# Kernel optimization log

Measured on AMD Instinct MI355X. Metric: run time of the kernel, lower is better.

Reference implementation:

```python
import jax, jax.numpy as jnp
import numpy as np

N_FEAT = 1024
N_HIDDEN = 31


def _lstm_cell(x, h, c, W_ih, W_hh, b_ih, b_hh):
    # PyTorch LSTMCell: gates ordered i, f, g, o
    gates = x @ W_ih.T + b_ih + h @ W_hh.T + b_hh
    i, f, g, o = jnp.split(gates, 4, axis=-1)
    i = jax.nn.sigmoid(i)
    f = jax.nn.sigmoid(f)
    g = jnp.tanh(g)
    o = jax.nn.sigmoid(o)
    c_new = f * c + i * g
    h_new = o * jnp.tanh(c_new)
    return h_new, c_new


def setup_inputs() -> dict:
    key = jax.random.key(0)
    ks = jax.random.split(key, 12)
    B, T = 64, 512
    s1 = 1.0 / np.sqrt(N_HIDDEN)
    inp = {
        "input": jax.random.normal(ks[0], (B, T, N_FEAT), dtype=jnp.float32),
        "W_ih1": jax.random.uniform(ks[1], (4 * N_HIDDEN, N_FEAT), jnp.float32, -s1, s1),
        "W_hh1": jax.random.uniform(ks[2], (4 * N_HIDDEN, N_HIDDEN), jnp.float32, -s1, s1),
        "b_ih1": jax.random.uniform(ks[3], (4 * N_HIDDEN,), jnp.float32, -s1, s1),
        "b_hh1": jax.random.uniform(ks[4], (4 * N_HIDDEN,), jnp.float32, -s1, s1),
        "W_ih2": jax.random.uniform(ks[5], (4 * N_HIDDEN, N_HIDDEN), jnp.float32, -s1, s1),
        "W_hh2": jax.random.uniform(ks[6], (4 * N_HIDDEN, N_HIDDEN), jnp.float32, -s1, s1),
        "b_ih2": jax.random.uniform(ks[7], (4 * N_HIDDEN,), jnp.float32, -s1, s1),
        "b_hh2": jax.random.uniform(ks[8], (4 * N_HIDDEN,), jnp.float32, -s1, s1),
        "W_lin": jax.random.uniform(ks[9], (N_FEAT, N_HIDDEN), jnp.float32, -s1, s1),
        "b_lin": jax.random.uniform(ks[10], (N_FEAT,), jnp.float32, -s1, s1),
        "future": 16,
    }
    return inp


def reference(input, W_ih1, W_hh1, b_ih1, b_hh1, W_ih2, W_hh2, b_ih2, b_hh2, W_lin, b_lin, future):
    B = input.shape[0]
    h0 = jnp.zeros((B, N_HIDDEN), dtype=input.dtype)
    state0 = (h0, h0, h0, h0)  # h_t, c_t, h_t2, c_t2

    def step(state, x_t):
        h_t, c_t, h_t2, c_t2 = state
        h_t, c_t = _lstm_cell(x_t, h_t, c_t, W_ih1, W_hh1, b_ih1, b_hh1)
        h_t2, c_t2 = _lstm_cell(h_t, h_t2, c_t2, W_ih2, W_hh2, b_ih2, b_hh2)
        out = h_t2 @ W_lin.T + b_lin  # [B, N_FEAT]
        return (h_t, c_t, h_t2, c_t2), out

    # teacher-forced pass over the given sequence
    xs = jnp.swapaxes(input, 0, 1)  # [T, B, F]
    state, outs = jax.lax.scan(step, state0, xs)
    last = outs[-1]

    def fut_step(carry, _):
        state, out = carry
        state, out = step(state, out)
        return (state, out), out

    if future > 0:
        _, fut_outs = jax.lax.scan(fut_step, (state, last), None, length=future)
        outs = jnp.concatenate([outs, fut_outs], axis=0)

    return jnp.swapaxes(outs, 0, 1)  # [B, T+future, N_FEAT]
```

## Files before the change

kernel.cpp:

```cpp
#include <hip/hip_runtime.h>
#include <hip/hip_bf16.h>

#define BB_  64
#define TT_  512
#define FF_  1024
#define HH_  31
#define GG_  124
#define FUT_ 16
#define TTOT_ 528
#define OUT_ROW_ ((size_t)TTOT_ * FF_)

#define PRE1_OFF ((size_t)0)
#define H2A_OFF  (PRE1_OFF + (size_t)TT_*64*128)
#define WT_OFF   (H2A_OFF  + (size_t)TTOT_*64*32)
#define MV_OFF   (WT_OFF   + 31*1024)

__device__ __forceinline__ float rdlane(float v, int k) {
    return __uint_as_float(__builtin_amdgcn_readlane(__float_as_uint(v), k));
}

#define REP31(M) M(0) M(1) M(2) M(3) M(4) M(5) M(6) M(7) M(8) M(9) \
                 M(10) M(11) M(12) M(13) M(14) M(15) M(16) M(17) M(18) M(19) \
                 M(20) M(21) M(22) M(23) M(24) M(25) M(26) M(27) M(28) M(29) M(30)
#define REP16E(M) M(0) M(2) M(4) M(6) M(8) M(10) M(12) M(14) \
                  M(16) M(18) M(20) M(22) M(24) M(26) M(28) M(30)
#define REP15O(M) M(1) M(3) M(5) M(7) M(9) M(11) M(13) M(15) \
                  M(17) M(19) M(21) M(23) M(25) M(27) M(29)

__global__ __launch_bounds__(256) void k_front(
    const float* __restrict__ X,
    const float* __restrict__ Wih1,
    const float* __restrict__ bih1,
    const float* __restrict__ bhh1,
    const float* __restrict__ Wlin,
    const float* __restrict__ blin,
    float* __restrict__ pre1,
    float* __restrict__ WT,
    float* __restrict__ Mv)
{
    __shared__ __align__(16) float xs[32][128];
    __shared__ __align__(16) float ws[32][128];
    const int blk = blockIdx.x;
    const int tid = threadIdx.x;

    if (blk < 256) {
        const int t0   = blk * 2;
        const int tcol = tid & 15, trow = tid >> 4;
        const int c0 = tcol * 8, r0 = trow * 8;

        float4 a0[8], a1[8];
#pragma unroll
        for (int r = 0; r < 8; r++) { a0[r] = make_float4(0.f,0.f,0.f,0.f); a1[r] = a0[r]; }

        for (int kc = 0; kc < 32; ++kc) {
            const int k0f = kc * 32;
#pragma unroll
            for (int p = 0; p < 4; p++) {
                int i = tid + p * 256;
                int r = i >> 3, f = i & 7;
                int bb = r & 63, tt = t0 + (r >> 6);
                float4 v = *(const float4*)(X + (size_t)bb * TT_ * FF_ + (size_t)tt * FF_ + k0f + f * 4);
                xs[f * 4 + 0][r] = v.x; xs[f * 4 + 1][r] = v.y;
                xs[f * 4 + 2][r] = v.z; xs[f * 4 + 3][r] = v.w;
            }
#pragma unroll
            for (int p = 0; p < 4; p++) {
                int i = tid + p * 256;
                int g = i >> 3, f = i & 7;
                float4 v = make_float4(0.f, 0.f, 0.f, 0.f);
                if (g < GG_) v = *(const float4*)(Wih1 + (size_t)g * FF_ + k0f + f * 4);
                ws[f * 4 + 0][g] = v.x; ws[f * 4 + 1][g] = v.y;
                ws[f * 4 + 2][g] = v.z; ws[f * 4 + 3][g] = v.w;
            }
            __syncthreads();
#pragma unroll
            for (int k = 0; k < 32; k++) {
                float4 wv0 = *(const float4*)&ws[k][c0];
                float4 wv1 = *(const float4*)&ws[k][c0 + 4];
                float4 xa  = *(const float4*)&xs[k][r0];
                float4 xb  = *(const float4*)&xs[k][r0 + 4];
                float rx[8] = {xa.x, xa.y, xa.z, xa.w, xb.x, xb.y, xb.z, xb.w};
#pragma unroll
                for (int r = 0; r < 8; r++) {
                    a0[r].x += rx[r] * wv0.x; a0[r].y += rx[r] * wv0.y;
                    a0[r].z += rx[r] * wv0.z; a0[r].w += rx[r] * wv0.w;
                    a1[r].x += rx[r] * wv1.x; a1[r].y += rx[r] * wv1.y;
                    a1[r].z += rx[r] * wv1.z; a1[r].w += rx[r] * wv1.w;
                }
            }
            __syncthreads();
        }
        float bias0[4], bias1[4];
#pragma unroll
        for (int cc = 0; cc < 4; cc++) {
            int c = c0 + cc;
            bias0[cc] = (c < GG_) ? (bih1[c] + bhh1[c]) : 0.0f;
            c = c0 + 4 + cc;
            bias1[cc] = (c < GG_) ? (bih1[c] + bhh1[c]) : 0.0f;
        }
#pragma unroll
        for (int r = 0; r < 8; r++) {
            int row = r0 + r;
            int m = (t0 + (row >> 6)) * 64 + (row & 63);
            float4 o0 = a0[r], o1 = a1[r];
            o0.x += bias0[0]; o0.y += bias0[1]; o0.z += bias0[2]; o0.w += bias0[3];
            o1.x += bias1[0]; o1.y += bias1[1]; o1.z += bias1[2]; o1.w += bias1[3];
            *(float4*)(pre1 + (size_t)m * 128 + c0)     = o0;
            *(float4*)(pre1 + (size_t)m * 128 + c0 + 4) = o1;
        }
    } else if (blk < 380) {
        int i = (blk - 256) * 256 + tid;
        int j = i / 31;
        int k = i - j * 31;
        WT[k * 1024 + j] = Wlin[i];
    } else {
        int idx = (blk - 380) * 256 + tid;
        if (idx < GG_ * 32) {
            int g = idx >> 5, k = idx & 31;
            const float* wr = Wih1 + (size_t)g * FF_;
            float acc = 0.0f;
            if (k < 31) {
#pragma unroll 8
                for (int j = 0; j < FF_; j++) acc += wr[j] * Wlin[j * 31 + k];
            } else {
#pragma unroll 8
                for (int j = 0; j < FF_; j++) acc += wr[j] * blin[j];
            }
            Mv[idx] = acc;
        }
    }
}

__global__ __attribute__((amdgpu_flat_work_group_size(128, 128), amdgpu_waves_per_eu(1)))
void k2_recur(
    const float* __restrict__ pre1,
    const float* __restrict__ Whh1,
    const float* __restrict__ Wih2,
    const float* __restrict__ Whh2,
    const float* __restrict__ bih1, const float* __restrict__ bhh1,
    const float* __restrict__ bih2, const float* __restrict__ bhh2,
    const float* __restrict__ Mv,
    float* __restrict__ h2a)
{
    __shared__ float gA[2][128];
    __shared__ float g2[2][128];
    const int L  = threadIdx.x;
    const int bb = blockIdx.x;
    const int j  = L & 63;
    const int gc = (L < GG_) ? L : (GG_ - 1);
    const bool isg = (gc >= 62 && gc < 93);
    const bool selhi = (j >= 32);
    const int sidx = selhi ? (j - 32) : j;

#define WLOAD(k) float w1_##k  = Whh1[gc * 31 + k]; \
                 float wi2_##k = Wih2[gc * 31 + k]; \
                 float wh2_##k = Whh2[gc * 31 + k];
    REP31(WLOAD)
#undef WLOAD
#define WPIN(k) asm("" : "+v"(w1_##k), "+v"(wi2_##k), "+v"(wh2_##k));
    REP31(WPIN)
#undef WPIN

    const float b2c = bih2[gc] + bhh2[gc];

    float hv = 0.0f, cv = 0.0f;

    float cur0 = pre1[(size_t)bb * 128 + L];
    float pnxt = pre1[((size_t)1 * 64 + bb) * 128 + L];
    float pnx2 = pre1[((size_t)2 * 64 + bb) * 128 + L];
    {
        float pa0 = cur0, pa1 = 0.0f;
#define DPE(k) { float hk = rdlane(hv, 32 + k); pa0 += w1_##k * hk; }
#define DPO(k) { float hk = rdlane(hv, 32 + k); pa1 += w1_##k * hk; }
        REP16E(DPE)
        REP15O(DPO)
#undef DPE
#undef DPO
        float a = pa0 + pa1;
        float z = isg ? (2.0f * a) : a;
        float s = 1.0f / (1.0f + __expf(-z));
        gA[1][L] = isg ? (2.0f * s - 1.0f) : s;
    }
    __syncthreads();
    {
        const float* gsrc = &gA[1][0];
        float ig = gsrc[sidx];
        float fg = gsrc[sidx + 31];
        float gg = gsrc[sidx + 62];
        float og = gsrc[sidx + 93];
        float cvn = fg * cv + ig * gg;
        float e = __expf(-2.0f * cvn);
        float hvn = og * (2.0f / (1.0f + e) - 1.0f);
        cv = selhi ? cvn : 0.0f;
        hv = selhi ? hvn : 0.0f;
    }

    for (int t = 0; t < TT_ - 1; t++) {
        const int pb = t & 1;
        const float cur = pnxt;
        pnxt = pnx2;
        if (t + 3 < TT_) pnx2 = pre1[((size_t)(t + 3) * 64 + bb) * 128 + L];

        float bi0 = b2c, bi1 = 0.0f, bh0 = 0.0f, bh1 = 0.0f;
        float pa0 = cur, pa1 = 0.0f;
#define DME(k) { float h1k = rdlane(hv, 32 + k); float h2k = rdlane(hv, k); \
                 bi0 += wi2_##k * h1k; bh0 += wh2_##k * h2k; pa0 += w1_##k * h1k; }
#define DMO(k) { float h1k = rdlane(hv, 32 + k); float h2k = rdlane(hv, k); \
                 bi1 += wi2_##k * h1k; bh1 += wh2_##k * h2k; pa1 += w1_##k * h1k; }
        REP16E(DME)
        REP15O(DMO)
#undef DME
#undef DMO
        float b = (bi0 + bi1) + (bh0 + bh1);
        float a = pa0 + pa1;
        {
            float z = isg ? (2.0f * b) : b;
            float s = 1.0f / (1.0f + __expf(-z));
            g2[pb][L] = isg ? (2.0f * s - 1.0f) : s;
        }
        {
            float z = isg ? (2.0f * a) : a;
            float s = 1.0f / (1.0f + __expf(-z));
            gA[pb][L] = isg ? (2.0f * s - 1.0f) : s;
        }
        __syncthreads();
        {
            const float* gsrc = selhi ? &gA[pb][0] : &g2[pb][0];
            float ig = gsrc[sidx];
            float fg = gsrc[sidx + 31];
            float gg = gsrc[sidx + 62];
            float og = gsrc[sidx + 93];
            cv = fg * cv + ig * gg;
            float e = __expf(-2.0f * cv);
            hv = og * (2.0f / (1.0f + e) - 1.0f);
        }
        if (L < HH_) h2a[((size_t)t * 64 + bb) * 32 + L] = hv;
    }

    {
        float bi0 = b2c, bi1 = 0.0f, bh0 = 0.0f, bh1 = 0.0f;
#define DTE(k) { float h1k = rdlane(hv, 32 + k); float h2k = rdlane(hv, k); \
                 bi0 += wi2_##k * h1k; bh0 += wh2_##k * h2k; }
#define DTO(k) { float h1k = rdlane(hv, 32 + k); float h2k = rdlane(hv, k); \
                 bi1 += wi2_##k * h1k; bh1 += wh2_##k * h2k; }
        REP16E(DTE)
        REP15O(DTO)
#undef DTE
#undef DTO
        float b = (bi0 + bi1) + (bh0 + bh1);
        float z = isg ? (2.0f * b) : b;
        float s = 1.0f / (1.0f + __expf(-z));
        g2[1][L] = isg ? (2.0f * s - 1.0f) : s;
    }
    __syncthreads();
    {
        const float* gsrc = &g2[1][0];
        float ig = gsrc[sidx];
        float fg = gsrc[sidx + 31];
        float gg = gsrc[sidx + 62];
        float og = gsrc[sidx + 93];
        float cvn = fg * cv + ig * gg;
        float e = __expf(-2.0f * cvn);
        float hvn = og * (2.0f / (1.0f + e) - 1.0f);
        cv = selhi ? cv : cvn;
        hv = selhi ? hv : hvn;
    }
    if (L < HH_) h2a[((size_t)(TT_ - 1) * 64 + bb) * 32 + L] = hv;

#define MLOAD(k) float m_##k = Mv[gc * 32 + k];
    REP31(MLOAD)
#undef MLOAD
    float m_31 = Mv[gc * 32 + 31];
#define MPIN(k) asm("" : "+v"(m_##k));
    REP31(MPIN)
#undef MPIN
    asm("" : "+v"(m_31));
    const float b1c = bih1[gc] + bhh1[gc];

    for (int sft = 0; sft < FUT_; sft++) {
        float pa0 = b1c + m_31, pa1 = 0.0f;
#define DFE(k) { float h2k = rdlane(hv, k); pa0 += m_##k * h2k; }
#define DFO(k) { float h2k = rdlane(hv, k); pa1 += m_##k * h2k; }
        REP16E(DFE)
        REP15O(DFO)
#undef DFE
#undef DFO
#define DGE(k) { float h1k = rdlane(hv, 32 + k); pa0 += w1_##k * h1k; }
#define DGO(k) { float h1k = rdlane(hv, 32 + k); pa1 += w1_##k * h1k; }
        REP16E(DGE)
        REP15O(DGO)
#undef DGE
#undef DGO
        {
            float a = pa0 + pa1;
            float z = isg ? (2.0f * a) : a;
            float s = 1.0f / (1.0f + __expf(-z));
            gA[0][L] = isg ? (2.0f * s - 1.0f) : s;
        }
        __syncthreads();
        {
            const float* gsrc = &gA[0][0];
            float ig = gsrc[sidx];
            float fg = gsrc[sidx + 31];
            float gg = gsrc[sidx + 62];
            float og = gsrc[sidx + 93];
            float cvn = fg * cv + ig * gg;
            float e = __expf(-2.0f * cvn);
            float hvn = og * (2.0f / (1.0f + e) - 1.0f);
            cv = selhi ? cvn : cv;
            hv = selhi ? hvn : hv;
        }
        float bi0 = b2c, bi1 = 0.0f, bh0 = 0.0f, bh1 = 0.0f;
#define DHE(k) { float h1k = rdlane(hv, 32 + k); float h2k = rdlane(hv, k); \
                 bi0 += wi2_##k * h1k; bh0 += wh2_##k * h2k; }
#define DHO(k) { float h1k = rdlane(hv, 32 + k); float h2k = rdlane(hv, k); \
                 bi1 += wi2_##k * h1k; bh1 += wh2_##k * h2k; }
        REP16E(DHE)
        REP15O(DHO)
#undef DHE
#undef DHO
        {
            float b = (bi0 + bi1) + (bh0 + bh1);
            float z = isg ? (2.0f * b) : b;
            float s = 1.0f / (1.0f + __expf(-z));
            g2[0][L] = isg ? (2.0f * s - 1.0f) : s;
        }
        __syncthreads();
        {
            const float* gsrc = &g2[0][0];
            float ig = gsrc[sidx];
            float fg = gsrc[sidx + 31];
            float gg = gsrc[sidx + 62];
            float og = gsrc[sidx + 93];
            float cvn = fg * cv + ig * gg;
            float e = __expf(-2.0f * cvn);
            float hvn = og * (2.0f / (1.0f + e) - 1.0f);
            cv = selhi ? cv : cvn;
            hv = selhi ? hv : hvn;
        }
        if (L < HH_) h2a[((size_t)(TT_ + sft) * 64 + bb) * 32 + L] = hv;
    }
}

__global__ __launch_bounds__(256) void k3_outlin(
    const float* __restrict__ h2a,
    const float* __restrict__ WT,
    const float* __restrict__ blin,
    float* __restrict__ out)
{
    __shared__ __align__(16) float hl[32][32];
    const int tid = threadIdx.x;
    const int m0  = blockIdx.x * 32;
#pragma unroll
    for (int p = 0; p < 4; p++) {
        int i = tid + p * 256;
        int r = i >> 5, k = i & 31;
        hl[r][k] = h2a[(size_t)(m0 + r) * 32 + k];
    }
    __syncthreads();
    const int c0 = tid * 4;
    float4 bl = *(const float4*)(blin + c0);
    float4 acc[32];
#pragma unroll
    for (int r = 0; r < 32; r++) acc[r] = bl;
    for (int k = 0; k < 31; k++) {
        float4 wv = *(const float4*)(WT + k * 1024 + c0);
#pragma unroll
        for (int r = 0; r < 32; r++) {
            float h = hl[r][k];
            acc[r].x += h * wv.x; acc[r].y += h * wv.y;
            acc[r].z += h * wv.z; acc[r].w += h * wv.w;
        }
    }
    const int t  = m0 >> 6;
    const int b0 = m0 & 63;
#pragma unroll
    for (int r = 0; r < 32; r++) {
        int b = b0 + r;
        *(float4*)(out + (size_t)b * OUT_ROW_ + (size_t)t * FF_ + c0) = acc[r];
    }
}

extern "C" void kernel_launch(void* const* d_in, const int* in_sizes, int n_in,
                              void* d_out, int out_size, void* d_ws, size_t ws_size,
                              hipStream_t stream) {
    (void)in_sizes; (void)n_in; (void)out_size; (void)ws_size;
    const float* X    = (const float*)d_in[0];
    const float* Wih1 = (const float*)d_in[1];
    const float* Whh1 = (const float*)d_in[2];
    const float* bih1 = (const float*)d_in[3];
    const float* bhh1 = (const float*)d_in[4];
    const float* Wih2 = (const float*)d_in[5];
    const float* Whh2 = (const float*)d_in[6];
    const float* bih2 = (const float*)d_in[7];
    const float* bhh2 = (const float*)d_in[8];
    const float* Wlin = (const float*)d_in[9];
    const float* blin = (const float*)d_in[10];

    float* ws   = (float*)d_ws;
    float* pre1 = ws + PRE1_OFF;
    float* h2a  = ws + H2A_OFF;
    float* WT   = ws + WT_OFF;
    float* Mv   = ws + MV_OFF;
    float* out  = (float*)d_out;

    hipLaunchKernelGGL(k_front,   dim3(396),    dim3(256), 0, stream,
                       X, Wih1, bih1, bhh1, Wlin, blin, pre1, WT, Mv);
    hipLaunchKernelGGL(k2_recur,  dim3(BB_),    dim3(128), 0, stream, pre1, Whh1, Wih2, Whh2,
                       bih1, bhh1, bih2, bhh2, Mv, h2a);
    hipLaunchKernelGGL(k3_outlin, dim3(TTOT_*2), dim3(256), 0, stream, h2a, WT, blin, out);
}
```

Before: 776.8 us.

## Fuse recurrence and output projection with flag-synchronized producer/consumer blocks

Merges the recurrent LSTM kernel and the output linear kernel into one launch. 64 producer blocks run the recurrence and bump per-64-timestep global counters, while 128 consumer blocks spin on those flags and compute output chunks as soon as their timesteps are ready. This lets the large output write overlap the serial recurrence instead of running after it. It also XOR-swizzles the shared-memory tiles in the front GEMM to cut bank conflicts. The cost is a spin-wait protocol that depends on all blocks being co-resident, an extra zeroing launch, and producer blocks doubling to 256 threads with idle half-waves running dummy barriers.

```diff
diff --git a/kernel.cpp b/kernel.cpp
--- a/kernel.cpp
+++ b/kernel.cpp
@@ -14,9 +14,20 @@
 #define H2A_OFF  (PRE1_OFF + (size_t)TT_*64*128)
 #define WT_OFF   (H2A_OFF  + (size_t)TTOT_*64*32)
 #define MV_OFF   (WT_OFF   + 31*1024)
+#define FLG_OFF  (MV_OFF   + 124*32)
+
+#define KBLK   64
+#define NCONS  128
+#define NCHUNK (TTOT_ * 2)
 
 __device__ __forceinline__ float rdlane(float v, int k) {
     return __uint_as_float(__builtin_amdgcn_readlane(__float_as_uint(v), k));
+}
+__device__ __forceinline__ int aload_acq(int* p) {
+    return __hip_atomic_load(p, __ATOMIC_ACQUIRE, __HIP_MEMORY_SCOPE_AGENT);
+}
+__device__ __forceinline__ void aadd_rel(int* p, int v) {
+    __hip_atomic_fetch_add(p, v, __ATOMIC_RELEASE, __HIP_MEMORY_SCOPE_AGENT);
 }
 
 #define REP31(M) M(0) M(1) M(2) M(3) M(4) M(5) M(6) M(7) M(8) M(9) \
@@ -26,6 +37,10 @@
                   M(16) M(18) M(20) M(22) M(24) M(26) M(28) M(30)
 #define REP15O(M) M(1) M(3) M(5) M(7) M(9) M(11) M(13) M(15) \
                   M(17) M(19) M(21) M(23) M(25) M(27) M(29)
+
+__global__ void k_zero(int* flg) {
+    if (threadIdx.x < 16) flg[threadIdx.x] = 0;
+}
 
 __global__ __launch_bounds__(256) void k_front(
     const float* __restrict__ X,
@@ -60,8 +75,9 @@
                 int r = i >> 3, f = i & 7;
                 int bb = r & 63, tt = t0 + (r >> 6);
                 float4 v = *(const float4*)(X + (size_t)bb * TT_ * FF_ + (size_t)tt * FF_ + k0f + f * 4);
-                xs[f * 4 + 0][r] = v.x; xs[f * 4 + 1][r] = v.y;
-                xs[f * 4 + 2][r] = v.z; xs[f * 4 + 3][r] = v.w;
+                const int sc = r ^ (f << 3);
+                xs[f * 4 + 0][sc] = v.x; xs[f * 4 + 1][sc] = v.y;
+                xs[f * 4 + 2][sc] = v.z; xs[f * 4 + 3][sc] = v.w;
             }
 #pragma unroll
             for (int p = 0; p < 4; p++) {
@@ -69,16 +85,20 @@
                 int g = i >> 3, f = i & 7;
                 float4 v = make_float4(0.f, 0.f, 0.f, 0.f);
                 if (g < GG_) v = *(const float4*)(Wih1 + (size_t)g * FF_ + k0f + f * 4);
-                ws[f * 4 + 0][g] = v.x; ws[f * 4 + 1][g] = v.y;
-                ws[f * 4 + 2][g] = v.z; ws[f * 4 + 3][g] = v.w;
+                const int sg = g ^ (f << 3);
+                ws[f * 4 + 0][sg] = v.x; ws[f * 4 + 1][sg] = v.y;
+                ws[f * 4 + 2][sg] = v.z; ws[f * 4 + 3][sg] = v.w;
             }
             __syncthreads();
 #pragma unroll
             for (int k = 0; k < 32; k++) {
-                float4 wv0 = *(const float4*)&ws[k][c0];
-                float4 wv1 = *(const float4*)&ws[k][c0 + 4];
-                float4 xa  = *(const float4*)&xs[k][r0];
-                float4 xb  = *(const float4*)&xs[k][r0 + 4];
+                const int xk = ((k >> 2) & 7) << 3;
+                const int cb = c0 ^ xk;
+                const int rb = r0 ^ xk;
+                float4 wv0 = *(const float4*)&ws[k][cb];
+                float4 wv1 = *(const float4*)&ws[k][cb + 4];
+                float4 xa  = *(const float4*)&xs[k][rb];
+                float4 xb  = *(const float4*)&xs[k][rb + 4];
                 float rx[8] = {xa.x, xa.y, xa.z, xa.w, xb.x, xb.y, xb.z, xb.w};
 #pragma unroll
                 for (int r = 0; r < 8; r++) {
@@ -131,8 +151,7 @@
     }
 }
 
-__global__ __attribute__((amdgpu_flat_work_group_size(128, 128), amdgpu_waves_per_eu(1)))
-void k2_recur(
+__global__ __launch_bounds__(256) void k_23(
     const float* __restrict__ pre1,
     const float* __restrict__ Whh1,
     const float* __restrict__ Wih2,
@@ -140,166 +159,110 @@
     const float* __restrict__ bih1, const float* __restrict__ bhh1,
     const float* __restrict__ bih2, const float* __restrict__ bhh2,
     const float* __restrict__ Mv,
-    float* __restrict__ h2a)
+    const float* __restrict__ WT,
+    const float* __restrict__ blin,
+    float* __restrict__ h2a,
+    float* __restrict__ out,
+    int*   __restrict__ flg)
 {
-    __shared__ float gA[2][128];
-    __shared__ float g2[2][128];
-    const int L  = threadIdx.x;
-    const int bb = blockIdx.x;
-    const int j  = L & 63;
-    const int gc = (L < GG_) ? L : (GG_ - 1);
-    const bool isg = (gc >= 62 && gc < 93);
-    const bool selhi = (j >= 32);
-    const int sidx = selhi ? (j - 32) : j;
+    __shared__ __align__(16) float smem[1024];
+    const int blk = blockIdx.x;
+    const int tid = threadIdx.x;
+
+    if (blk >= KBLK) {
+        float (*hl)[32] = (float(*)[32])smem;
+        const int cid = blk - KBLK;
+        int gseen = 0;
+        for (int c = cid; c < NCHUNK; c += NCONS) {
+            const int m0 = c * 32;
+            const int t  = m0 >> 6;
+            const int g  = (t < TT_) ? (t >> 6) : 8;
+            while (gseen <= g) {
+                if (aload_acq(&flg[gseen]) == KBLK) gseen++;
+                else __builtin_amdgcn_s_sleep(8);
+            }
+#pragma unroll
+            for (int p = 0; p < 4; p++) {
+                int i = tid + p * 256;
+                int r = i >> 5, k = i & 31;
+                hl[r][k] = h2a[(size_t)(m0 + r) * 32 + k];
+            }
+            __syncthreads();
+            const int c0 = tid * 4;
+            float4 bl = *(const float4*)(blin + c0);
+            float4 acc[32];
+#pragma unroll
+            for (int r = 0; r < 32; r++) acc[r] = bl;
+            for (int k = 0; k < 31; k++) {
+                float4 wv = *(const float4*)(WT + k * 1024 + c0);
+#pragma unroll
+                for (int r = 0; r < 32; r++) {
+                    float h = hl[r][k];
+                    acc[r].x += h * wv.x; acc[r].y += h * wv.y;
+                    acc[r].z += h * wv.z; acc[r].w += h * wv.w;
+                }
+            }
+            const int b0 = m0 & 63;
+#pragma unroll
+            for (int r = 0; r < 32; r++) {
+                int b = b0 + r;
+                *(float4*)(out + (size_t)b * OUT_ROW_ + (size_t)t * FF_ + c0) = acc[r];
+            }
+            __syncthreads();
+        }
+        return;
+    }
+
+    if (tid >= 128) {
+        __syncthreads();
+        for (int t = 0; t < TT_ - 1; t++) __syncthreads();
+        __syncthreads();
+        for (int s = 0; s < FUT_; s++) { __syncthreads(); __syncthreads(); }
+        return;
+    }
+
+    {
+        const int L  = tid;
+        const int bb = blk;
+        const int j  = L & 63;
+        const int gc = (L < GG_) ? L : (GG_ - 1);
+        const bool isg = (gc >= 62 && gc < 93);
+        const bool selhi = (j >= 32);
+        const int sidx = selhi ? (j - 32) : j;
+        float (*gA)[128] = (float(*)[128])smem;
+        float (*g2)[128] = (float(*)[128])(smem + 256);
 
 #define WLOAD(k) float w1_##k  = Whh1[gc * 31 + k]; \
                  float wi2_##k = Wih2[gc * 31 + k]; \
                  float wh2_##k = Whh2[gc * 31 + k];
-    REP31(WLOAD)
+        REP31(WLOAD)
 #undef WLOAD
 #define WPIN(k) asm("" : "+v"(w1_##k), "+v"(wi2_##k), "+v"(wh2_##k));
-    REP31(WPIN)
+        REP31(WPIN)
 #undef WPIN
 
-    const float b2c = bih2[gc] + bhh2[gc];
-
-    float hv = 0.0f, cv = 0.0f;
-
-    float cur0 = pre1[(size_t)bb * 128 + L];
-    float pnxt = pre1[((size_t)1 * 64 + bb) * 128 + L];
-    float pnx2 = pre1[((size_t)2 * 64 + bb) * 128 + L];
-    {
-        float pa0 = cur0, pa1 = 0.0f;
+        const float b2c = bih2[gc] + bhh2[gc];
+        float hv = 0.0f, cv = 0.0f;
+
+        float cur0 = pre1[(size_t)bb * 128 + L];
+        float pnxt = pre1[((size_t)1 * 64 + bb) * 128 + L];
+        float pnx2 = pre1[((size_t)2 * 64 + bb) * 128 + L];
+        {
+            float pa0 = cur0, pa1 = 0.0f;
 #define DPE(k) { float hk = rdlane(hv, 32 + k); pa0 += w1_##k * hk; }
 #define DPO(k) { float hk = rdlane(hv, 32 + k); pa1 += w1_##k * hk; }
-        REP16E(DPE)
-        REP15O(DPO)
+            REP16E(DPE)
+            REP15O(DPO)
 #undef DPE
 #undef DPO
-        float a = pa0 + pa1;
-        float z = isg ? (2.0f * a) : a;
-        float s = 1.0f / (1.0f + __expf(-z));
-        gA[1][L] = isg ? (2.0f * s - 1.0f) : s;
-    }
-    __syncthreads();
-    {
-        const float* gsrc = &gA[1][0];
-        float ig = gsrc[sidx];
-        float fg = gsrc[sidx + 31];
-        float gg = gsrc[sidx + 62];
-        float og = gsrc[sidx + 93];
-        float cvn = fg * cv + ig * gg;
-        float e = __expf(-2.0f * cvn);
-        float hvn = og * (2.0f / (1.0f + e) - 1.0f);
-        cv = selhi ? cvn : 0.0f;
-        hv = selhi ? hvn : 0.0f;
-    }
-
-    for (int t = 0; t < TT_ - 1; t++) {
-        const int pb = t & 1;
-        const float cur = pnxt;
-        pnxt = pnx2;
-        if (t + 3 < TT_) pnx2 = pre1[((size_t)(t + 3) * 64 + bb) * 128 + L];
-
-        float bi0 = b2c, bi1 = 0.0f, bh0 = 0.0f, bh1 = 0.0f;
-        float pa0 = cur, pa1 = 0.0f;
-#define DME(k) { float h1k = rdlane(hv, 32 + k); float h2k = rdlane(hv, k); \
-                 bi0 += wi2_##k * h1k; bh0 += wh2_##k * h2k; pa0 += w1_##k * h1k; }
-#define DMO(k) { float h1k = rdlane(hv, 32 + k); float h2k = rdlane(hv, k); \
-                 bi1 += wi2_##k * h1k; bh1 += wh2_##k * h2k; pa1 += w1_##k * h1k; }
-        REP16E(DME)
-        REP15O(DMO)
-#undef DME
-#undef DMO
-        float b = (bi0 + bi1) + (bh0 + bh1);
-        float a = pa0 + pa1;
-        {
-            float z = isg ? (2.0f * b) : b;
-            float s = 1.0f / (1.0f + __expf(-z));
-            g2[pb][L] = isg ? (2.0f * s - 1.0f) : s;
-        }
-        {
-            float z = isg ? (2.0f * a) : a;
-            float s = 1.0f / (1.0f + __expf(-z));
-            gA[pb][L] = isg ? (2.0f * s - 1.0f) : s;
-        }
-        __syncthreads();
-        {
-            const float* gsrc = selhi ? &gA[pb][0] : &g2[pb][0];
-            float ig = gsrc[sidx];
-            float fg = gsrc[sidx + 31];
-            float gg = gsrc[sidx + 62];
-            float og = gsrc[sidx + 93];
-            cv = fg * cv + ig * gg;
-            float e = __expf(-2.0f * cv);
-            hv = og * (2.0f / (1.0f + e) - 1.0f);
-        }
-        if (L < HH_) h2a[((size_t)t * 64 + bb) * 32 + L] = hv;
-    }
-
-    {
-        float bi0 = b2c, bi1 = 0.0f, bh0 = 0.0f, bh1 = 0.0f;
-#define DTE(k) { float h1k = rdlane(hv, 32 + k); float h2k = rdlane(hv, k); \
-                 bi0 += wi2_##k * h1k; bh0 += wh2_##k * h2k; }
-#define DTO(k) { float h1k = rdlane(hv, 32 + k); float h2k = rdlane(hv, k); \
-                 bi1 += wi2_##k * h1k; bh1 += wh2_##k * h2k; }
-        REP16E(DTE)
-        REP15O(DTO)
-#undef DTE
-#undef DTO
-        float b = (bi0 + bi1) + (bh0 + bh1);
-        float z = isg ? (2.0f * b) : b;
-        float s = 1.0f / (1.0f + __expf(-z));
-        g2[1][L] = isg ? (2.0f * s - 1.0f) : s;
-    }
-    __syncthreads();
-    {
-        const float* gsrc = &g2[1][0];
-        float ig = gsrc[sidx];
-        float fg = gsrc[sidx + 31];
-        float gg = gsrc[sidx + 62];
-        float og = gsrc[sidx + 93];
-        float cvn = fg * cv + ig * gg;
-        float e = __expf(-2.0f * cvn);
-        float hvn = og * (2.0f / (1.0f + e) - 1.0f);
-        cv = selhi ? cv : cvn;
-        hv = selhi ? hv : hvn;
-    }
-    if (L < HH_) h2a[((size_t)(TT_ - 1) * 64 + bb) * 32 + L] = hv;
-
-#define MLOAD(k) float m_##k = Mv[gc * 32 + k];
-    REP31(MLOAD)
-#undef MLOAD
-    float m_31 = Mv[gc * 32 + 31];
-#define MPIN(k) asm("" : "+v"(m_##k));
-    REP31(MPIN)
-#undef MPIN
-    asm("" : "+v"(m_31));
-    const float b1c = bih1[gc] + bhh1[gc];
-
-    for (int sft = 0; sft < FUT_; sft++) {
-        float pa0 = b1c + m_31, pa1 = 0.0f;
-#define DFE(k) { float h2k = rdlane(hv, k); pa0 += m_##k * h2k; }
-#define DFO(k) { float h2k = rdlane(hv, k); pa1 += m_##k * h2k; }
-        REP16E(DFE)
-        REP15O(DFO)
-#undef DFE
-#undef DFO
-#define DGE(k) { float h1k = rdlane(hv, 32 + k); pa0 += w1_##k * h1k; }
-#define DGO(k) { float h1k = rdlane(hv, 32 + k); pa1 += w1_##k * h1k; }
-        REP16E(DGE)
-        REP15O(DGO)
-#undef DGE
-#undef DGO
-        {
             float a = pa0 + pa1;
             float z = isg ? (2.0f * a) : a;
             float s = 1.0f / (1.0f + __expf(-z));
-            gA[0][L] = isg ? (2.0f * s - 1.0f) : s;
+            gA[1][L] = isg ? (2.0f * s - 1.0f) : s;
         }
         __syncthreads();
         {
-            const float* gsrc = &gA[0][0];
+            const float* gsrc = &gA[1][0];
             float ig = gsrc[sidx];
             float fg = gsrc[sidx + 31];
             float gg = gsrc[sidx + 62];
@@ -307,27 +270,71 @@
             float cvn = fg * cv + ig * gg;
             float e = __expf(-2.0f * cvn);
             float hvn = og * (2.0f / (1.0f + e) - 1.0f);
-            cv = selhi ? cvn : cv;
-            hv = selhi ? hvn : hv;
-        }
-        float bi0 = b2c, bi1 = 0.0f, bh0 = 0.0f, bh1 = 0.0f;
-#define DHE(k) { float h1k = rdlane(hv, 32 + k); float h2k = rdlane(hv, k); \
+            cv = selhi ? cvn : 0.0f;
+            hv = selhi ? hvn : 0.0f;
+        }
+
+        for (int t = 0; t < TT_ - 1; t++) {
+            const int pb = t & 1;
+            const float cur = pnxt;
+            pnxt = pnx2;
+            if (t + 3 < TT_) pnx2 = pre1[((size_t)(t + 3) * 64 + bb) * 128 + L];
+
+            float bi0 = b2c, bi1 = 0.0f, bh0 = 0.0f, bh1 = 0.0f;
+            float pa0 = cur, pa1 = 0.0f;
+#define DME(k) { float h1k = rdlane(hv, 32 + k); float h2k = rdlane(hv, k); \
+                 bi0 += wi2_##k * h1k; bh0 += wh2_##k * h2k; pa0 += w1_##k * h1k; }
+#define DMO(k) { float h1k = rdlane(hv, 32 + k); float h2k = rdlane(hv, k); \
+                 bi1 += wi2_##k * h1k; bh1 += wh2_##k * h2k; pa1 += w1_##k * h1k; }
+            REP16E(DME)
+            REP15O(DMO)
+#undef DME
+#undef DMO
+            float b = (bi0 + bi1) + (bh0 + bh1);
+            float a = pa0 + pa1;
+            {
+                float z = isg ? (2.0f * b) : b;
+                float s = 1.0f / (1.0f + __expf(-z));
+                g2[pb][L] = isg ? (2.0f * s - 1.0f) : s;
+            }
+            {
+                float z = isg ? (2.0f * a) : a;
+                float s = 1.0f / (1.0f + __expf(-z));
+                gA[pb][L] = isg ? (2.0f * s - 1.0f) : s;
+            }
+            __syncthreads();
+            {
+                const float* gsrc = selhi ? &gA[pb][0] : &g2[pb][0];
+                float ig = gsrc[sidx];
+                float fg = gsrc[sidx + 31];
+                float gg = gsrc[sidx + 62];
+                float og = gsrc[sidx + 93];
+                cv = fg * cv + ig * gg;
+                float e = __expf(-2.0f * cv);
+                hv = og * (2.0f / (1.0f + e) - 1.0f);
+            }
+            if (L < HH_) h2a[((size_t)t * 64 + bb) * 32 + L] = hv;
+            if (((t & 63) == 63) && L == 0) aadd_rel(&flg[t >> 6], 1);
+        }
+
+        {
+            float bi0 = b2c, bi1 = 0.0f, bh0 = 0.0f, bh1 = 0.0f;
+#define DTE(k) { float h1k = rdlane(hv, 32 + k); float h2k = rdlane(hv, k); \
                  bi0 += wi2_##k * h1k; bh0 += wh2_##k * h2k; }
-#define DHO(k) { float h1k = rdlane(hv, 32 + k); float h2k = rdlane(hv, k); \
+#define DTO(k) { float h1k = rdlane(hv, 32 + k); float h2k = rdlane(hv, k); \
                  bi1 += wi2_##k * h1k; bh1 += wh2_##k * h2k; }
-        REP16E(DHE)
-        REP15O(DHO)
-#undef DHE
-#undef DHO
-        {
+            REP16E(DTE)
+            REP15O(DTO)
+#undef DTE
+#undef DTO
             float b = (bi0 + bi1) + (bh0 + bh1);
             float z = isg ? (2.0f * b) : b;
             float s = 1.0f / (1.0f + __expf(-z));
-            g2[0][L] = isg ? (2.0f * s - 1.0f) : s;
+            g2[1][L] = isg ? (2.0f * s - 1.0f) : s;
         }
         __syncthreads();
         {
-            const float* gsrc = &g2[0][0];
+            const float* gsrc = &g2[1][0];
             float ig = gsrc[sidx];
             float fg = gsrc[sidx + 31];
             float gg = gsrc[sidx + 62];
@@ -338,46 +345,83 @@
             cv = selhi ? cv : cvn;
             hv = selhi ? hv : hvn;
         }
-        if (L < HH_) h2a[((size_t)(TT_ + sft) * 64 + bb) * 32 + L] = hv;
-    }
-}
-
-__global__ __launch_bounds__(256) void k3_outlin(
-    const float* __restrict__ h2a,
-    const float* __restrict__ WT,
-    const float* __restrict__ blin,
-    float* __restrict__ out)
-{
-    __shared__ __align__(16) float hl[32][32];
-    const int tid = threadIdx.x;
-    const int m0  = blockIdx.x * 32;
-#pragma unroll
-    for (int p = 0; p < 4; p++) {
-        int i = tid + p * 256;
-        int r = i >> 5, k = i & 31;
-        hl[r][k] = h2a[(size_t)(m0 + r) * 32 + k];
-    }
-    __syncthreads();
-    const int c0 = tid * 4;
-    float4 bl = *(const float4*)(blin + c0);
-    float4 acc[32];
-#pragma unroll
-    for (int r = 0; r < 32; r++) acc[r] = bl;
-    for (int k = 0; k < 31; k++) {
-        float4 wv = *(const float4*)(WT + k * 1024 + c0);
-#pragma unroll
-        for (int r = 0; r < 32; r++) {
-            float h = hl[r][k];
-            acc[r].x += h * wv.x; acc[r].y += h * wv.y;
-            acc[r].z += h * wv.z; acc[r].w += h * wv.w;
-        }
-    }
-    const int t  = m0 >> 6;
-    const int b0 = m0 & 63;
-#pragma unroll
-    for (int r = 0; r < 32; r++) {
-        int b = b0 + r;
-        *(float4*)(out + (size_t)b * OUT_ROW_ + (size_t)t * FF_ + c0) = acc[r];
+        if (L < HH_) h2a[((size_t)(TT_ - 1) * 64 + bb) * 32 + L] = hv;
+        if (L == 0) aadd_rel(&flg[7], 1);
+
+#define MLOAD(k) float m_##k = Mv[gc * 32 + k];
+        REP31(MLOAD)
+#undef MLOAD
+        float m_31 = Mv[gc * 32 + 31];
+#define MPIN(k) asm("" : "+v"(m_##k));
+        REP31(MPIN)
+#undef MPIN
+        asm("" : "+v"(m_31));
+        const float b1c = bih1[gc] + bhh1[gc];
+
+        for (int sft = 0; sft < FUT_; sft++) {
+            float pa0 = b1c + m_31, pa1 = 0.0f;
+#define DFE(k) { float h2k = rdlane(hv, k); pa0 += m_##k * h2k; }
+#define DFO(k) { float h2k = rdlane(hv, k); pa1 += m_##k * h2k; }
+            REP16E(DFE)
+            REP15O(DFO)
+#undef DFE
+#undef DFO
+#define DGE(k) { float h1k = rdlane(hv, 32 + k); pa0 += w1_##k * h1k; }
+#define DGO(k) { float h1k = rdlane(hv, 32 + k); pa1 += w1_##k * h1k; }
+            REP16E(DGE)
+            REP15O(DGO)
+#undef DGE
+#undef DGO
+            {
+                float a = pa0 + pa1;
+                float z = isg ? (2.0f * a) : a;
+                float s = 1.0f / (1.0f + __expf(-z));
+                gA[0][L] = isg ? (2.0f * s - 1.0f) : s;
+            }
+            __syncthreads();
+            {
+                const float* gsrc = &gA[0][0];
+                float ig = gsrc[sidx];
+                float fg = gsrc[sidx + 31];
+                float gg = gsrc[sidx + 62];
+                float og = gsrc[sidx + 93];
+                float cvn = fg * cv + ig * gg;
+                float e = __expf(-2.0f * cvn);
+                float hvn = og * (2.0f / (1.0f + e) - 1.0f);
+                cv = selhi ? cvn : cv;
+                hv = selhi ? hvn : hv;
+            }
+            float bi0 = b2c, bi1 = 0.0f, bh0 = 0.0f, bh1 = 0.0f;
+#define DHE(k) { float h1k = rdlane(hv, 32 + k); float h2k = rdlane(hv, k); \
+                 bi0 += wi2_##k * h1k; bh0 += wh2_##k * h2k; }
+#define DHO(k) { float h1k = rdlane(hv, 32 + k); float h2k = rdlane(hv, k); \
+                 bi1 += wi2_##k * h1k; bh1 += wh2_##k * h2k; }
+            REP16E(DHE)
+            REP15O(DHO)
+#undef DHE
+#undef DHO
+            {
+                float b = (bi0 + bi1) + (bh0 + bh1);
+                float z = isg ? (2.0f * b) : b;
+                float s = 1.0f / (1.0f + __expf(-z));
+                g2[0][L] = isg ? (2.0f * s - 1.0f) : s;
+            }
+            __syncthreads();
+            {
+                const float* gsrc = &g2[0][0];
+                float ig = gsrc[sidx];
+                float fg = gsrc[sidx + 31];
+                float gg = gsrc[sidx + 62];
+                float og = gsrc[sidx + 93];
+                float cvn = fg * cv + ig * gg;
+                float e = __expf(-2.0f * cvn);
+                float hvn = og * (2.0f / (1.0f + e) - 1.0f);
+                cv = selhi ? cv : cvn;
+                hv = selhi ? hv : hvn;
+            }
+            if (L < HH_) h2a[((size_t)(TT_ + sft) * 64 + bb) * 32 + L] = hv;
+        }
+        if (L == 0) aadd_rel(&flg[8], 1);
     }
 }
 
@@ -402,11 +446,13 @@
     float* h2a  = ws + H2A_OFF;
     float* WT   = ws + WT_OFF;
     float* Mv   = ws + MV_OFF;
+    int*   flg  = (int*)(ws + FLG_OFF);
     float* out  = (float*)d_out;
 
-    hipLaunchKernelGGL(k_front,   dim3(396),    dim3(256), 0, stream,
+    hipLaunchKernelGGL(k_zero,  dim3(1),   dim3(64),  0, stream, flg);
+    hipLaunchKernelGGL(k_front, dim3(396), dim3(256), 0, stream,
                        X, Wih1, bih1, bhh1, Wlin, blin, pre1, WT, Mv);
-    hipLaunchKernelGGL(k2_recur,  dim3(BB_),    dim3(128), 0, stream, pre1, Whh1, Wih2, Whh2,
-                       bih1, bhh1, bih2, bhh2, Mv, h2a);
-    hipLaunchKernelGGL(k3_outlin, dim3(TTOT_*2), dim3(256), 0, stream, h2a, WT, blin, out);
-}
+    hipLaunchKernelGGL(k_23, dim3(KBLK + NCONS), dim3(256), 0, stream,
+                       pre1, Whh1, Wih2, Whh2, bih1, bhh1, bih2, bhh2,
+                       Mv, WT, blin, h2a, out, flg);
+}
```

New measurement: 1.103 ms. +42.0%, slower.

## Replace LDS-tiled input projection GEMM with per-row register dot products

Applied to the files above, without the earlier changes.

The input-projection GEMM in k_front no longer stages X and W_ih1 tiles in shared memory. Each thread now owns one (t,b) row and half of the 124 gates, and accumulates 62 dot products in registers while streaming its X row with a one-step prefetch. The weight loads are wave-uniform, so they can be served as scalar or broadcast loads, and the block-wide syncs are gone. The costs are heavy register pressure (62 accumulators plus weights), which lowers occupancy, and uncoalesced X loads, since each lane reads a different 4 KB row.

```diff
diff --git a/kernel.cpp b/kernel.cpp
--- a/kernel.cpp
+++ b/kernel.cpp
@@ -38,75 +38,41 @@
     float* __restrict__ WT,
     float* __restrict__ Mv)
 {
-    __shared__ __align__(16) float xs[32][128];
-    __shared__ __align__(16) float ws[32][128];
     const int blk = blockIdx.x;
     const int tid = threadIdx.x;
 
     if (blk < 256) {
-        const int t0   = blk * 2;
-        const int tcol = tid & 15, trow = tid >> 4;
-        const int c0 = tcol * 8, r0 = trow * 8;
-
-        float4 a0[8], a1[8];
-#pragma unroll
-        for (int r = 0; r < 8; r++) { a0[r] = make_float4(0.f,0.f,0.f,0.f); a1[r] = a0[r]; }
-
-        for (int kc = 0; kc < 32; ++kc) {
-            const int k0f = kc * 32;
-#pragma unroll
-            for (int p = 0; p < 4; p++) {
-                int i = tid + p * 256;
-                int r = i >> 3, f = i & 7;
-                int bb = r & 63, tt = t0 + (r >> 6);
-                float4 v = *(const float4*)(X + (size_t)bb * TT_ * FF_ + (size_t)tt * FF_ + k0f + f * 4);
-                xs[f * 4 + 0][r] = v.x; xs[f * 4 + 1][r] = v.y;
-                xs[f * 4 + 2][r] = v.z; xs[f * 4 + 3][r] = v.w;
+        const int lrow = tid & 127;
+        const int m    = blk * 128 + lrow;
+        const int t    = m >> 6, b = m & 63;
+        const int g0   = __builtin_amdgcn_readfirstlane((tid >> 7) * 62);
+        const float* xrow  = X + (size_t)b * TT_ * FF_ + (size_t)t * FF_;
+        const float* wbase = Wih1 + (size_t)g0 * FF_;
+
+        float acc[62];
+#pragma unroll
+        for (int g = 0; g < 62; g++) acc[g] = 0.0f;
+
+        float4 xv = *(const float4*)(xrow);
+        for (int kc = 0; kc < FF_; kc += 4) {
+            const float4 xc = xv;
+            const int kn = (kc + 4 < FF_) ? (kc + 4) : 0;
+            xv = *(const float4*)(xrow + kn);
+#pragma unroll
+            for (int g = 0; g < 62; g++) {
+                float4 wv = *(const float4*)(wbase + (size_t)g * FF_ + kc);
+                acc[g] += xc.x * wv.x;
+                acc[g] += xc.y * wv.y;
+                acc[g] += xc.z * wv.z;
+                acc[g] += xc.w * wv.w;
             }
-#pragma unroll
-            for (int p = 0; p < 4; p++) {
-                int i = tid + p * 256;
-                int g = i >> 3, f = i & 7;
-                float4 v = make_float4(0.f, 0.f, 0.f, 0.f);
-                if (g < GG_) v = *(const float4*)(Wih1 + (size_t)g * FF_ + k0f + f * 4);
-                ws[f * 4 + 0][g] = v.x; ws[f * 4 + 1][g] = v.y;
-                ws[f * 4 + 2][g] = v.z; ws[f * 4 + 3][g] = v.w;
-            }
-            __syncthreads();
-#pragma unroll
-            for (int k = 0; k < 32; k++) {
-                float4 wv0 = *(const float4*)&ws[k][c0];
-                float4 wv1 = *(const float4*)&ws[k][c0 + 4];
-                float4 xa  = *(const float4*)&xs[k][r0];
-                float4 xb  = *(const float4*)&xs[k][r0 + 4];
-                float rx[8] = {xa.x, xa.y, xa.z, xa.w, xb.x, xb.y, xb.z, xb.w};
-#pragma unroll
-                for (int r = 0; r < 8; r++) {
-                    a0[r].x += rx[r] * wv0.x; a0[r].y += rx[r] * wv0.y;
-                    a0[r].z += rx[r] * wv0.z; a0[r].w += rx[r] * wv0.w;
-                    a1[r].x += rx[r] * wv1.x; a1[r].y += rx[r] * wv1.y;
-                    a1[r].z += rx[r] * wv1.z; a1[r].w += rx[r] * wv1.w;
-                }
-            }
-            __syncthreads();
-        }
-        float bias0[4], bias1[4];
-#pragma unroll
-        for (int cc = 0; cc < 4; cc++) {
-            int c = c0 + cc;
-            bias0[cc] = (c < GG_) ? (bih1[c] + bhh1[c]) : 0.0f;
-            c = c0 + 4 + cc;
-            bias1[cc] = (c < GG_) ? (bih1[c] + bhh1[c]) : 0.0f;
-        }
-#pragma unroll
-        for (int r = 0; r < 8; r++) {
-            int row = r0 + r;
-            int m = (t0 + (row >> 6)) * 64 + (row & 63);
-            float4 o0 = a0[r], o1 = a1[r];
-            o0.x += bias0[0]; o0.y += bias0[1]; o0.z += bias0[2]; o0.w += bias0[3];
-            o1.x += bias1[0]; o1.y += bias1[1]; o1.z += bias1[2]; o1.w += bias1[3];
-            *(float4*)(pre1 + (size_t)m * 128 + c0)     = o0;
-            *(float4*)(pre1 + (size_t)m * 128 + c0 + 4) = o1;
+        }
+#pragma unroll
+        for (int g = 0; g < 62; g++) {
+            pre1[(size_t)m * 128 + g0 + g] = acc[g] + (bih1[g0 + g] + bhh1[g0 + g]);
+        }
+        if (tid < 128) {
+            *(float4*)(pre1 + (size_t)m * 128 + 124) = make_float4(0.f, 0.f, 0.f, 0.f);
         }
     } else if (blk < 380) {
         int i = (blk - 256) * 256 + tid;
@@ -404,9 +370,9 @@
     float* Mv   = ws + MV_OFF;
     float* out  = (float*)d_out;
 
-    hipLaunchKernelGGL(k_front,   dim3(396),    dim3(256), 0, stream,
+    hipLaunchKernelGGL(k_front,   dim3(396),     dim3(256), 0, stream,
                        X, Wih1, bih1, bhh1, Wlin, blin, pre1, WT, Mv);
-    hipLaunchKernelGGL(k2_recur,  dim3(BB_),    dim3(128), 0, stream, pre1, Whh1, Wih2, Whh2,
+    hipLaunchKernelGGL(k2_recur,  dim3(BB_),     dim3(128), 0, stream, pre1, Whh1, Wih2, Whh2,
                        bih1, bhh1, bih2, bhh2, Mv, h2a);
     hipLaunchKernelGGL(k3_outlin, dim3(TTOT_*2), dim3(256), 0, stream, h2a, WT, blin, out);
 }
```

After: 1.344 ms. +73.0%, slower.
